# Kernel optimization log

Measured on AMD Instinct MI355X. Metric: run time of the kernel, lower is better.

Reference implementation:

```python
import jax, jax.numpy as jnp
import numpy as np

L, B, S, D = 12, 2, 2048, 768
QK, H, V = 128, 512, 32000
SCALE = 128 ** (-0.5)


def setup_inputs() -> dict:
    key = jax.random.key(0)
    ks = jax.random.split(key, 11)
    p = lambda k, shp: jax.random.normal(k, shp, dtype=jnp.float32) * 0.02
    return {
        "layer_outputs": jax.random.normal(ks[0], (L, B, S, D), dtype=jnp.float32),
        "Wq": p(ks[1], (D, QK)), "bq": jnp.zeros((QK,), jnp.float32),
        "Wk": p(ks[2], (D, QK)), "bk": jnp.zeros((QK,), jnp.float32),
        "Wv": p(ks[3], (D, H)),  "bv": jnp.zeros((H,), jnp.float32),
        "W1": p(ks[4], (H, H // 2)), "b1": jnp.zeros((H // 2,), jnp.float32),
        "W2": p(ks[5], (H // 2, V)), "b2": jnp.zeros((V,), jnp.float32),
    }


def reference(layer_outputs, Wq, bq, Wk, bk, Wv, bv, W1, b1, W2, b2):
    # layer_outputs: (L, B, S, D) -> h: (S, L, B, D) as in torch permute(2,0,1,3)
    h = jnp.transpose(layer_outputs, (2, 0, 1, 3))
    q_in = h.mean(axis=1)                              # (S, B, D)
    q = jax.nn.relu(q_in @ Wq + bq)                    # (S, B, 128)
    k = jax.nn.relu(h @ Wk + bk)                       # (S, L, B, 128)
    scores = jnp.einsum('sbd,slbd->slb', q, k)[..., None] * SCALE  # (S, L, B, 1)
    attn = jax.nn.softmax(scores, axis=1)              # softmax over layer axis
    v = h @ Wv + bv                                    # (S, L, B, H)
    agg = jnp.sum(attn * v, axis=1)                    # (S, B, H)
    agg = jnp.transpose(agg, (1, 0, 2))                # (B, S, H)
    mid = jax.nn.relu(agg @ W1 + b1)                   # (B, S, H//2); dropout is eval-mode identity
    return mid @ W2 + b2                               # (B, S, V)
```

## Files before the change

kernel.cpp:

```cpp
#include <hip/hip_runtime.h>

#define Snum 2048
#define SCALE 0.08838834764831845f

typedef __attribute__((ext_vector_type(8))) __bf16 bf16x8;
typedef __attribute__((ext_vector_type(4))) float f32x4;

__device__ inline unsigned short f2bf(float f) {
    unsigned int u = __float_as_uint(f);
    unsigned int r = u + 0x7FFFu + ((u >> 16) & 1u);
    return (unsigned short)(r >> 16);
}
__device__ inline float bf2f(unsigned short u) {
    return __uint_as_float(((unsigned)u) << 16);
}
__device__ inline void gld_lds16(const unsigned short* g, unsigned short* l) {
    __builtin_amdgcn_global_load_lds(
        (const __attribute__((address_space(1))) unsigned int*)g,
        (__attribute__((address_space(3))) unsigned int*)l, 16, 0, 0);
}

__global__ __launch_bounds__(256) void transpose_f2bf(
    const float* __restrict__ in, unsigned short* __restrict__ out, int K, int N)
{
    __shared__ float t[32][33];
    const int bx = blockIdx.x;
    const int by = blockIdx.y;
    const int tx = threadIdx.x & 31, ty = threadIdx.x >> 5;
    #pragma unroll
    for (int i = 0; i < 4; ++i) {
        int k = by * 32 + ty + i * 8, n = bx * 32 + tx;
        t[ty + i * 8][tx] = in[(size_t)k * N + n];
    }
    __syncthreads();
    #pragma unroll
    for (int i = 0; i < 4; ++i) {
        int n = bx * 32 + ty + i * 8, k = by * 32 + tx;
        out[(size_t)n * K + k] = f2bf(t[tx][ty + i * 8]);
    }
}

__global__ __launch_bounds__(256) void proj_qk(
    const float* __restrict__ x, const unsigned short* __restrict__ Bt,
    const float* __restrict__ bk,
    unsigned short* __restrict__ Kall,
    unsigned short* __restrict__ Pq)
{
    __shared__ __align__(16) unsigned short As[2][64 * 32];
    __shared__ __align__(16) unsigned short Bs[2][256 * 32];
    const int tid = threadIdx.x;
    const int wid = tid >> 6, lane = tid & 63;
    const int wn = wid * 64;
    const int lr = lane & 15, g = lane >> 4;
    const int r0 = blockIdx.x * 64;
    const int K = 768, NT = K / 32;

    const int arow = tid >> 2, akc = (tid & 3) * 8;

    f32x4 acc[4][4] = {};

    float4 a0 = *(const float4*)(x + (size_t)(r0 + arow) * K + akc);
    float4 a1 = *(const float4*)(x + (size_t)(r0 + arow) * K + akc + 4);
    {
        unsigned short v[8];
        v[0] = f2bf(a0.x); v[1] = f2bf(a0.y); v[2] = f2bf(a0.z); v[3] = f2bf(a0.w);
        v[4] = f2bf(a1.x); v[5] = f2bf(a1.y); v[6] = f2bf(a1.z); v[7] = f2bf(a1.w);
        *(uint4*)&As[0][arow * 32 + akc] = *(uint4*)v;
    }
    #pragma unroll
    for (int c = 0; c < 4; ++c) {
        int rr = wid * 64 + c * 16;
        gld_lds16(Bt + (size_t)(rr + (lane >> 2)) * K + (lane & 3) * 8, &Bs[0][rr * 32]);
    }
    __syncthreads();

    for (int t = 0; t < NT; ++t) {
        const int cur = t & 1, nxt = cur ^ 1;
        if (t + 1 < NT) {
            const int k0 = (t + 1) * 32;
            a0 = *(const float4*)(x + (size_t)(r0 + arow) * K + k0 + akc);
            a1 = *(const float4*)(x + (size_t)(r0 + arow) * K + k0 + akc + 4);
            #pragma unroll
            for (int c = 0; c < 4; ++c) {
                int rr = wid * 64 + c * 16;
                gld_lds16(Bt + (size_t)(rr + (lane >> 2)) * K + k0 + (lane & 3) * 8,
                          &Bs[nxt][rr * 32]);
            }
        }

        bf16x8 aF[4], bF[4];
        #pragma unroll
        for (int mm = 0; mm < 4; ++mm) aF[mm] = *(const bf16x8*)&As[cur][(mm * 16 + lr) * 32 + g * 8];
        #pragma unroll
        for (int nn = 0; nn < 4; ++nn) bF[nn] = *(const bf16x8*)&Bs[cur][(wn + nn * 16 + lr) * 32 + g * 8];
        #pragma unroll
        for (int mm = 0; mm < 4; ++mm)
            #pragma unroll
            for (int nn = 0; nn < 4; ++nn)
                acc[mm][nn] = __builtin_amdgcn_mfma_f32_16x16x32_bf16(aF[mm], bF[nn], acc[mm][nn], 0, 0, 0);

        if (t + 1 < NT) {
            unsigned short v[8];
            v[0] = f2bf(a0.x); v[1] = f2bf(a0.y); v[2] = f2bf(a0.z); v[3] = f2bf(a0.w);
            v[4] = f2bf(a1.x); v[5] = f2bf(a1.y); v[6] = f2bf(a1.z); v[7] = f2bf(a1.w);
            *(uint4*)&As[nxt][arow * 32 + akc] = *(uint4*)v;
        }
        __syncthreads();
    }

    #pragma unroll
    for (int mm = 0; mm < 4; ++mm)
        #pragma unroll
        for (int nn = 0; nn < 4; ++nn) {
            int col = wn + nn * 16 + lr;
            #pragma unroll
            for (int reg = 0; reg < 4; ++reg) {
                int orow = r0 + mm * 16 + g * 4 + reg;
                float v = acc[mm][nn][reg];
                if (col < 128) {
                    float kv = v + bk[col];
                    Kall[(size_t)orow * 128 + col] = f2bf(kv > 0.f ? kv : 0.f);
                } else {
                    Pq[(size_t)orow * 128 + (col - 128)] = f2bf(v);
                }
            }
        }
}

__global__ __launch_bounds__(256) void scores_hbar(
    const float* __restrict__ x,
    const unsigned short* __restrict__ Pq,
    const float* __restrict__ bq,
    const unsigned short* __restrict__ Kall,
    unsigned short* __restrict__ hbar)
{
    const int wid = threadIdx.x >> 6, lane = threadIdx.x & 63;
    const int r = blockIdx.x * 4 + wid;
    const int b = r >> 11, s = r & 2047;

    float qa = 0.f, qb_ = 0.f;
    #pragma unroll
    for (int l = 0; l < 12; ++l) {
        const unsigned short* prow = Pq + ((size_t)(l * 2 + b) * Snum + s) * 128 + lane * 2;
        unsigned int u = *(const unsigned int*)prow;
        qa += bf2f((unsigned short)(u & 0xFFFF));
        qb_ += bf2f((unsigned short)(u >> 16));
    }
    float q0 = qa * (1.0f / 12.0f) + bq[lane * 2];
    float q1 = qb_ * (1.0f / 12.0f) + bq[lane * 2 + 1];
    q0 = q0 > 0.f ? q0 : 0.f;
    q1 = q1 > 0.f ? q1 : 0.f;
    q0 = bf2f(f2bf(q0)); q1 = bf2f(f2bf(q1));

    float sc[12];
    #pragma unroll
    for (int l = 0; l < 12; ++l) {
        const unsigned short* krow = Kall + ((size_t)(l * 2 + b) * Snum + s) * 128 + lane * 2;
        unsigned int u = *(const unsigned int*)krow;
        float p = q0 * bf2f((unsigned short)(u & 0xFFFF)) + q1 * bf2f((unsigned short)(u >> 16));
        #pragma unroll
        for (int off = 32; off > 0; off >>= 1) p += __shfl_xor(p, off, 64);
        sc[l] = p * SCALE;
    }
    float m = sc[0];
    #pragma unroll
    for (int l = 1; l < 12; ++l) m = fmaxf(m, sc[l]);
    float att[12], den = 0.f;
    #pragma unroll
    for (int l = 0; l < 12; ++l) { att[l] = __expf(sc[l] - m); den += att[l]; }
    const float inv = 1.0f / den;
    #pragma unroll
    for (int l = 0; l < 12; ++l) att[l] *= inv;

    #pragma unroll
    for (int jv = 0; jv < 3; ++jv) {
        const int d0 = jv * 256 + lane * 4;
        float a0 = 0.f, a1 = 0.f, a2 = 0.f, a3 = 0.f;
        #pragma unroll
        for (int l = 0; l < 12; ++l) {
            const float4 v = *(const float4*)(x + ((size_t)(l * 2 + b) * Snum + s) * 768 + d0);
            a0 += att[l] * v.x; a1 += att[l] * v.y; a2 += att[l] * v.z; a3 += att[l] * v.w;
        }
        ushort4 o;
        o.x = f2bf(a0); o.y = f2bf(a1); o.z = f2bf(a2); o.w = f2bf(a3);
        *(ushort4*)(hbar + (size_t)r * 768 + d0) = o;
    }
}

template <int RELU, int OUT_BF16>
__global__ __launch_bounds__(256) void gemm64(
    const unsigned short* __restrict__ A, const unsigned short* __restrict__ Bt,
    const float* __restrict__ bias, void* __restrict__ out, int M, int N, int K)
{
    __shared__ __align__(16) unsigned short As[64][40];
    __shared__ __align__(16) unsigned short Bs[64][40];
    const int tid = threadIdx.x;
    const int bn = blockIdx.x, bm = blockIdx.y;
    const int wid = tid >> 6, lane = tid & 63;
    const int wm = (wid >> 1) * 32, wn = (wid & 1) * 32;
    const int lr = lane & 15, g = lane >> 4;
    const int r0 = bm * 64, c0 = bn * 64;

    f32x4 acc[2][2] = {};
    const int row = tid >> 2, kc = (tid & 3) * 8;

    for (int k0 = 0; k0 < K; k0 += 32) {
        __syncthreads();
        *(uint4*)&As[row][kc] = *(const uint4*)(A  + (size_t)(r0 + row) * K + k0 + kc);
        *(uint4*)&Bs[row][kc] = *(const uint4*)(Bt + (size_t)(c0 + row) * K + k0 + kc);
        __syncthreads();

        bf16x8 aF[2], bF[2];
        #pragma unroll
        for (int mm = 0; mm < 2; ++mm) aF[mm] = *(const bf16x8*)&As[wm + mm * 16 + lr][g * 8];
        #pragma unroll
        for (int nn = 0; nn < 2; ++nn) bF[nn] = *(const bf16x8*)&Bs[wn + nn * 16 + lr][g * 8];
        #pragma unroll
        for (int mm = 0; mm < 2; ++mm)
            #pragma unroll
            for (int nn = 0; nn < 2; ++nn)
                acc[mm][nn] = __builtin_amdgcn_mfma_f32_16x16x32_bf16(aF[mm], bF[nn], acc[mm][nn], 0, 0, 0);
    }

    #pragma unroll
    for (int mm = 0; mm < 2; ++mm)
        #pragma unroll
        for (int nn = 0; nn < 2; ++nn) {
            int col = c0 + wn + nn * 16 + lr;
            float bcol = bias[col];
            #pragma unroll
            for (int reg = 0; reg < 4; ++reg) {
                int orow = r0 + wm + mm * 16 + g * 4 + reg;
                float v = acc[mm][nn][reg] + bcol;
                if (RELU) v = v > 0.f ? v : 0.f;
                if (OUT_BF16) ((unsigned short*)out)[(size_t)orow * N + col] = f2bf(v);
                else          ((float*)out)[(size_t)orow * N + col] = v;
            }
        }
}

__global__ __launch_bounds__(256) void gemm_out(
    const unsigned short* __restrict__ A,
    const unsigned short* __restrict__ Bt,
    const float* __restrict__ bias, float* __restrict__ out)
{
    __shared__ __align__(16) unsigned short As[2][128 * 32];
    __shared__ __align__(16) unsigned short Bs[2][128 * 32];
    const int K = 256, N = 32000, NT = K / 32;
    const int orig = blockIdx.x;
    const int swz = (orig & 7) * 1000 + (orig >> 3);
    const int bn = swz >> 5;
    const int bm = swz & 31;
    const int tid = threadIdx.x;
    const int wid = tid >> 6, lane = tid & 63;
    const int wm = (wid >> 1) * 64, wn = (wid & 1) * 64;
    const int lr = lane & 15, g = lane >> 4;
    const int r0 = bm * 128, c0 = bn * 128;

    f32x4 acc[4][4] = {};

    #pragma unroll
    for (int c = 0; c < 2; ++c) {
        int rr = wid * 32 + c * 16;
        gld_lds16(A  + (size_t)(r0 + rr + (lane >> 2)) * K + (lane & 3) * 8, &As[0][rr * 32]);
        gld_lds16(Bt + (size_t)(c0 + rr + (lane >> 2)) * K + (lane & 3) * 8, &Bs[0][rr * 32]);
    }
    __syncthreads();

    for (int t = 0; t < NT; ++t) {
        const int cur = t & 1, nxt = cur ^ 1;
        if (t + 1 < NT) {
            const int k0 = (t + 1) * 32;
            #pragma unroll
            for (int c = 0; c < 2; ++c) {
                int rr = wid * 32 + c * 16;
                gld_lds16(A  + (size_t)(r0 + rr + (lane >> 2)) * K + k0 + (lane & 3) * 8, &As[nxt][rr * 32]);
                gld_lds16(Bt + (size_t)(c0 + rr + (lane >> 2)) * K + k0 + (lane & 3) * 8, &Bs[nxt][rr * 32]);
            }
        }

        bf16x8 aF[4], bF[4];
        #pragma unroll
        for (int mm = 0; mm < 4; ++mm) aF[mm] = *(const bf16x8*)&As[cur][(wm + mm * 16 + lr) * 32 + g * 8];
        #pragma unroll
        for (int nn = 0; nn < 4; ++nn) bF[nn] = *(const bf16x8*)&Bs[cur][(wn + nn * 16 + lr) * 32 + g * 8];
        #pragma unroll
        for (int mm = 0; mm < 4; ++mm)
            #pragma unroll
            for (int nn = 0; nn < 4; ++nn)
                acc[mm][nn] = __builtin_amdgcn_mfma_f32_16x16x32_bf16(aF[mm], bF[nn], acc[mm][nn], 0, 0, 0);
        __syncthreads();
    }

    #pragma unroll
    for (int mm = 0; mm < 4; ++mm)
        #pragma unroll
        for (int nn = 0; nn < 4; ++nn) {
            int col = c0 + wn + nn * 16 + lr;
            float bcol = bias[col];
            #pragma unroll
            for (int reg = 0; reg < 4; ++reg) {
                int orow = r0 + wm + mm * 16 + g * 4 + reg;
                out[(size_t)orow * N + col] = acc[mm][nn][reg] + bcol;
            }
        }
}

extern "C" void kernel_launch(void* const* d_in, const int* in_sizes, int n_in,
                              void* d_out, int out_size, void* d_ws, size_t ws_size,
                              hipStream_t stream) {
    (void)in_sizes; (void)n_in; (void)out_size; (void)ws_size;

    const float* x  = (const float*)d_in[0];
    const float* Wq = (const float*)d_in[1];
    const float* bq = (const float*)d_in[2];
    const float* Wk = (const float*)d_in[3];
    const float* bk = (const float*)d_in[4];
    const float* Wv = (const float*)d_in[5];
    const float* bv = (const float*)d_in[6];
    const float* W1 = (const float*)d_in[7];
    const float* b1 = (const float*)d_in[8];
    const float* W2 = (const float*)d_in[9];
    const float* b2 = (const float*)d_in[10];

    char* p = (char*)d_ws;
    unsigned short* Wqkt  = (unsigned short*)p; p += (size_t)256 * 768 * 2;
    unsigned short* Wvt   = (unsigned short*)p; p += (size_t)512 * 768 * 2;
    unsigned short* W1t   = (unsigned short*)p; p += (size_t)256 * 512 * 2;
    unsigned short* W2t   = (unsigned short*)p; p += (size_t)32000 * 256 * 2;
    unsigned short* Kall  = (unsigned short*)p; p += (size_t)49152 * 128 * 2;
    unsigned short* Pq    = (unsigned short*)p; p += (size_t)49152 * 128 * 2;
    unsigned short* hbar  = (unsigned short*)p; p += (size_t)4096 * 768 * 2;
    unsigned short* aggb  = (unsigned short*)p; p += (size_t)4096 * 512 * 2;
    unsigned short* midb  = (unsigned short*)p; p += (size_t)4096 * 256 * 2;

    transpose_f2bf<<<dim3(128 / 32, 768 / 32), dim3(256), 0, stream>>>(Wk, Wqkt, 768, 128);
    transpose_f2bf<<<dim3(128 / 32, 768 / 32), dim3(256), 0, stream>>>(Wq, Wqkt + (size_t)128 * 768, 768, 128);
    transpose_f2bf<<<dim3(512 / 32, 768 / 32), dim3(256), 0, stream>>>(Wv, Wvt, 768, 512);
    transpose_f2bf<<<dim3(256 / 32, 512 / 32), dim3(256), 0, stream>>>(W1, W1t, 512, 256);
    transpose_f2bf<<<dim3(32000 / 32, 256 / 32), dim3(256), 0, stream>>>(W2, W2t, 256, 32000);

    proj_qk<<<dim3(49152 / 64), dim3(256), 0, stream>>>(x, Wqkt, bk, Kall, Pq);

    scores_hbar<<<dim3(1024), dim3(256), 0, stream>>>(x, Pq, bq, Kall, hbar);

    gemm64<0, 1><<<dim3(512 / 64, 4096 / 64), dim3(256), 0, stream>>>(
        hbar, Wvt, bv, aggb, 4096, 512, 768);

    gemm64<1, 1><<<dim3(256 / 64, 4096 / 64), dim3(256), 0, stream>>>(
        aggb, W1t, b1, midb, 4096, 256, 512);

    gemm_out<<<dim3(8000), dim3(256), 0, stream>>>(midb, W2t, b2, (float*)d_out);
}
```

Measured before the change: 340.2 us.

## Merge weight transposes, swizzle LDS, swap MFMA operands for vector stores, deepen gemm_out K tile

Merges the five weight transpose launches into a single kernel that dispatches on block index. It XOR-swizzles the LDS layouts in proj_qk and gemm_out to reduce bank conflicts on fragment reads. Swapping the MFMA operand order makes each lane hold four consecutive output columns, so the epilogues write ushort4/float4 vectors instead of scalars. gemm_out also moves to a 64-wide K tile with four iterations, which doubles its LDS footprint and may lower occupancy.

```diff
diff --git a/kernel.cpp b/kernel.cpp
--- a/kernel.cpp
+++ b/kernel.cpp
@@ -20,12 +20,22 @@
         (__attribute__((address_space(3))) unsigned int*)l, 16, 0, 0);
 }
 
-__global__ __launch_bounds__(256) void transpose_f2bf(
-    const float* __restrict__ in, unsigned short* __restrict__ out, int K, int N)
+__global__ __launch_bounds__(256) void transpose_all(
+    const float* __restrict__ W2, unsigned short* __restrict__ W2t,
+    const float* __restrict__ Wv, unsigned short* __restrict__ Wvt,
+    const float* __restrict__ W1, unsigned short* __restrict__ W1t,
+    const float* __restrict__ Wk, const float* __restrict__ Wq,
+    unsigned short* __restrict__ Wqkt)
 {
     __shared__ float t[32][33];
-    const int bx = blockIdx.x;
-    const int by = blockIdx.y;
+    const int id = blockIdx.x;
+    const float* in; unsigned short* out; int K, N, bx, by;
+    if (id < 8000)      { in = W2; out = W2t;  K = 256; N = 32000; by = id & 7;  bx = id >> 3; }
+    else if (id < 8384) { int q = id - 8000; in = Wv; out = Wvt;  K = 768; N = 512; bx = q & 15; by = q >> 4; }
+    else if (id < 8512) { int q = id - 8384; in = W1; out = W1t;  K = 512; N = 256; bx = q & 7;  by = q >> 3; }
+    else if (id < 8608) { int q = id - 8512; in = Wk; out = Wqkt; K = 768; N = 128; bx = q & 3;  by = q >> 2; }
+    else                { int q = id - 8608; in = Wq; out = Wqkt + (size_t)128 * 768; K = 768; N = 128; bx = q & 3; by = q >> 2; }
+
     const int tx = threadIdx.x & 31, ty = threadIdx.x >> 5;
     #pragma unroll
     for (int i = 0; i < 4; ++i) {
@@ -55,22 +65,24 @@
     const int r0 = blockIdx.x * 64;
     const int K = 768, NT = K / 32;
 
-    const int arow = tid >> 2, akc = (tid & 3) * 8;
+    const int arow = tid >> 2;
+    const int aslot = (tid & 3) ^ (arow & 3);
+    const int bslot = (lane & 3) ^ ((lane >> 2) & 3);
 
     f32x4 acc[4][4] = {};
 
-    float4 a0 = *(const float4*)(x + (size_t)(r0 + arow) * K + akc);
-    float4 a1 = *(const float4*)(x + (size_t)(r0 + arow) * K + akc + 4);
+    float4 a0 = *(const float4*)(x + (size_t)(r0 + arow) * K + (tid & 3) * 8);
+    float4 a1 = *(const float4*)(x + (size_t)(r0 + arow) * K + (tid & 3) * 8 + 4);
     {
         unsigned short v[8];
         v[0] = f2bf(a0.x); v[1] = f2bf(a0.y); v[2] = f2bf(a0.z); v[3] = f2bf(a0.w);
         v[4] = f2bf(a1.x); v[5] = f2bf(a1.y); v[6] = f2bf(a1.z); v[7] = f2bf(a1.w);
-        *(uint4*)&As[0][arow * 32 + akc] = *(uint4*)v;
+        *(uint4*)&As[0][arow * 32 + aslot * 8] = *(uint4*)v;
     }
     #pragma unroll
     for (int c = 0; c < 4; ++c) {
         int rr = wid * 64 + c * 16;
-        gld_lds16(Bt + (size_t)(rr + (lane >> 2)) * K + (lane & 3) * 8, &Bs[0][rr * 32]);
+        gld_lds16(Bt + (size_t)(rr + (lane >> 2)) * K + bslot * 8, &Bs[0][rr * 32]);
     }
     __syncthreads();
 
@@ -78,32 +90,32 @@
         const int cur = t & 1, nxt = cur ^ 1;
         if (t + 1 < NT) {
             const int k0 = (t + 1) * 32;
-            a0 = *(const float4*)(x + (size_t)(r0 + arow) * K + k0 + akc);
-            a1 = *(const float4*)(x + (size_t)(r0 + arow) * K + k0 + akc + 4);
+            a0 = *(const float4*)(x + (size_t)(r0 + arow) * K + k0 + (tid & 3) * 8);
+            a1 = *(const float4*)(x + (size_t)(r0 + arow) * K + k0 + (tid & 3) * 8 + 4);
             #pragma unroll
             for (int c = 0; c < 4; ++c) {
                 int rr = wid * 64 + c * 16;
-                gld_lds16(Bt + (size_t)(rr + (lane >> 2)) * K + k0 + (lane & 3) * 8,
-                          &Bs[nxt][rr * 32]);
+                gld_lds16(Bt + (size_t)(rr + (lane >> 2)) * K + k0 + bslot * 8, &Bs[nxt][rr * 32]);
             }
         }
 
         bf16x8 aF[4], bF[4];
-        #pragma unroll
-        for (int mm = 0; mm < 4; ++mm) aF[mm] = *(const bf16x8*)&As[cur][(mm * 16 + lr) * 32 + g * 8];
-        #pragma unroll
-        for (int nn = 0; nn < 4; ++nn) bF[nn] = *(const bf16x8*)&Bs[cur][(wn + nn * 16 + lr) * 32 + g * 8];
+        const int rslot = (g ^ (lr & 3)) * 8;
+        #pragma unroll
+        for (int mm = 0; mm < 4; ++mm) aF[mm] = *(const bf16x8*)&As[cur][(mm * 16 + lr) * 32 + rslot];
+        #pragma unroll
+        for (int nn = 0; nn < 4; ++nn) bF[nn] = *(const bf16x8*)&Bs[cur][(wn + nn * 16 + lr) * 32 + rslot];
         #pragma unroll
         for (int mm = 0; mm < 4; ++mm)
             #pragma unroll
             for (int nn = 0; nn < 4; ++nn)
-                acc[mm][nn] = __builtin_amdgcn_mfma_f32_16x16x32_bf16(aF[mm], bF[nn], acc[mm][nn], 0, 0, 0);
+                acc[mm][nn] = __builtin_amdgcn_mfma_f32_16x16x32_bf16(bF[nn], aF[mm], acc[mm][nn], 0, 0, 0);
 
         if (t + 1 < NT) {
             unsigned short v[8];
             v[0] = f2bf(a0.x); v[1] = f2bf(a0.y); v[2] = f2bf(a0.z); v[3] = f2bf(a0.w);
             v[4] = f2bf(a1.x); v[5] = f2bf(a1.y); v[6] = f2bf(a1.z); v[7] = f2bf(a1.w);
-            *(uint4*)&As[nxt][arow * 32 + akc] = *(uint4*)v;
+            *(uint4*)&As[nxt][arow * 32 + aslot * 8] = *(uint4*)v;
         }
         __syncthreads();
     }
@@ -112,17 +124,20 @@
     for (int mm = 0; mm < 4; ++mm)
         #pragma unroll
         for (int nn = 0; nn < 4; ++nn) {
-            int col = wn + nn * 16 + lr;
-            #pragma unroll
-            for (int reg = 0; reg < 4; ++reg) {
-                int orow = r0 + mm * 16 + g * 4 + reg;
-                float v = acc[mm][nn][reg];
-                if (col < 128) {
-                    float kv = v + bk[col];
-                    Kall[(size_t)orow * 128 + col] = f2bf(kv > 0.f ? kv : 0.f);
-                } else {
-                    Pq[(size_t)orow * 128 + (col - 128)] = f2bf(v);
+            const int row = r0 + mm * 16 + lr;
+            const int colb = wn + nn * 16 + g * 4;
+            unsigned short o[4];
+            if (colb < 128) {
+                #pragma unroll
+                for (int reg = 0; reg < 4; ++reg) {
+                    float kv = acc[mm][nn][reg] + bk[colb + reg];
+                    o[reg] = f2bf(kv > 0.f ? kv : 0.f);
                 }
+                *(ushort4*)&Kall[(size_t)row * 128 + colb] = *(ushort4*)o;
+            } else {
+                #pragma unroll
+                for (int reg = 0; reg < 4; ++reg) o[reg] = f2bf(acc[mm][nn][reg]);
+                *(ushort4*)&Pq[(size_t)row * 128 + (colb - 128)] = *(ushort4*)o;
             }
         }
 }
@@ -219,22 +234,28 @@
         for (int mm = 0; mm < 2; ++mm)
             #pragma unroll
             for (int nn = 0; nn < 2; ++nn)
-                acc[mm][nn] = __builtin_amdgcn_mfma_f32_16x16x32_bf16(aF[mm], bF[nn], acc[mm][nn], 0, 0, 0);
+                acc[mm][nn] = __builtin_amdgcn_mfma_f32_16x16x32_bf16(bF[nn], aF[mm], acc[mm][nn], 0, 0, 0);
     }
 
     #pragma unroll
     for (int mm = 0; mm < 2; ++mm)
         #pragma unroll
         for (int nn = 0; nn < 2; ++nn) {
-            int col = c0 + wn + nn * 16 + lr;
-            float bcol = bias[col];
+            const int orow = r0 + wm + mm * 16 + lr;
+            const int colb = c0 + wn + nn * 16 + g * 4;
+            float vr[4];
             #pragma unroll
             for (int reg = 0; reg < 4; ++reg) {
-                int orow = r0 + wm + mm * 16 + g * 4 + reg;
-                float v = acc[mm][nn][reg] + bcol;
-                if (RELU) v = v > 0.f ? v : 0.f;
-                if (OUT_BF16) ((unsigned short*)out)[(size_t)orow * N + col] = f2bf(v);
-                else          ((float*)out)[(size_t)orow * N + col] = v;
+                float v = acc[mm][nn][reg] + bias[colb + reg];
+                vr[reg] = (RELU && v < 0.f) ? 0.f : v;
+            }
+            if (OUT_BF16) {
+                unsigned short o[4];
+                #pragma unroll
+                for (int reg = 0; reg < 4; ++reg) o[reg] = f2bf(vr[reg]);
+                *(ushort4*)&((unsigned short*)out)[(size_t)orow * N + colb] = *(ushort4*)o;
+            } else {
+                *(float4*)&((float*)out)[(size_t)orow * N + colb] = *(float4*)vr;
             }
         }
 }
@@ -244,51 +265,58 @@
     const unsigned short* __restrict__ Bt,
     const float* __restrict__ bias, float* __restrict__ out)
 {
-    __shared__ __align__(16) unsigned short As[2][128 * 32];
-    __shared__ __align__(16) unsigned short Bs[2][128 * 32];
-    const int K = 256, N = 32000, NT = K / 32;
+    __shared__ __align__(16) unsigned short As[2][128 * 64];
+    __shared__ __align__(16) unsigned short Bs[2][128 * 64];
+    const int K = 256, N = 32000, NT = 4;
     const int orig = blockIdx.x;
     const int swz = (orig & 7) * 1000 + (orig >> 3);
-    const int bn = swz >> 5;
-    const int bm = swz & 31;
+    const int bn = swz >> 5, bm = swz & 31;
     const int tid = threadIdx.x;
     const int wid = tid >> 6, lane = tid & 63;
     const int wm = (wid >> 1) * 64, wn = (wid & 1) * 64;
     const int lr = lane & 15, g = lane >> 4;
     const int r0 = bm * 128, c0 = bn * 128;
 
+    const int srow = lane >> 3;
+    const int kslot = (lane & 7) ^ (srow & 7);
+
     f32x4 acc[4][4] = {};
 
     #pragma unroll
-    for (int c = 0; c < 2; ++c) {
-        int rr = wid * 32 + c * 16;
-        gld_lds16(A  + (size_t)(r0 + rr + (lane >> 2)) * K + (lane & 3) * 8, &As[0][rr * 32]);
-        gld_lds16(Bt + (size_t)(c0 + rr + (lane >> 2)) * K + (lane & 3) * 8, &Bs[0][rr * 32]);
+    for (int c = 0; c < 4; ++c) {
+        const int rb = wid * 32 + c * 8;
+        gld_lds16(A  + (size_t)(r0 + rb + srow) * K + kslot * 8, &As[0][rb * 64]);
+        gld_lds16(Bt + (size_t)(c0 + rb + srow) * K + kslot * 8, &Bs[0][rb * 64]);
     }
     __syncthreads();
 
     for (int t = 0; t < NT; ++t) {
         const int cur = t & 1, nxt = cur ^ 1;
         if (t + 1 < NT) {
-            const int k0 = (t + 1) * 32;
-            #pragma unroll
-            for (int c = 0; c < 2; ++c) {
-                int rr = wid * 32 + c * 16;
-                gld_lds16(A  + (size_t)(r0 + rr + (lane >> 2)) * K + k0 + (lane & 3) * 8, &As[nxt][rr * 32]);
-                gld_lds16(Bt + (size_t)(c0 + rr + (lane >> 2)) * K + k0 + (lane & 3) * 8, &Bs[nxt][rr * 32]);
-            }
-        }
-
-        bf16x8 aF[4], bF[4];
-        #pragma unroll
-        for (int mm = 0; mm < 4; ++mm) aF[mm] = *(const bf16x8*)&As[cur][(wm + mm * 16 + lr) * 32 + g * 8];
-        #pragma unroll
-        for (int nn = 0; nn < 4; ++nn) bF[nn] = *(const bf16x8*)&Bs[cur][(wn + nn * 16 + lr) * 32 + g * 8];
-        #pragma unroll
-        for (int mm = 0; mm < 4; ++mm)
+            const int k0 = (t + 1) * 64;
+            #pragma unroll
+            for (int c = 0; c < 4; ++c) {
+                const int rb = wid * 32 + c * 8;
+                gld_lds16(A  + (size_t)(r0 + rb + srow) * K + k0 + kslot * 8, &As[nxt][rb * 64]);
+                gld_lds16(Bt + (size_t)(c0 + rb + srow) * K + k0 + kslot * 8, &Bs[nxt][rb * 64]);
+            }
+        }
+
+        #pragma unroll
+        for (int kk = 0; kk < 2; ++kk) {
+            bf16x8 aF[4], bF[4];
+            #pragma unroll
+            for (int mm = 0; mm < 4; ++mm)
+                aF[mm] = *(const bf16x8*)&As[cur][(wm + mm * 16 + lr) * 64 + (((kk * 4 + g) ^ (lr & 7)) * 8)];
             #pragma unroll
             for (int nn = 0; nn < 4; ++nn)
-                acc[mm][nn] = __builtin_amdgcn_mfma_f32_16x16x32_bf16(aF[mm], bF[nn], acc[mm][nn], 0, 0, 0);
+                bF[nn] = *(const bf16x8*)&Bs[cur][(wn + nn * 16 + lr) * 64 + (((kk * 4 + g) ^ (lr & 7)) * 8)];
+            #pragma unroll
+            for (int mm = 0; mm < 4; ++mm)
+                #pragma unroll
+                for (int nn = 0; nn < 4; ++nn)
+                    acc[mm][nn] = __builtin_amdgcn_mfma_f32_16x16x32_bf16(bF[nn], aF[mm], acc[mm][nn], 0, 0, 0);
+        }
         __syncthreads();
     }
 
@@ -296,13 +324,15 @@
     for (int mm = 0; mm < 4; ++mm)
         #pragma unroll
         for (int nn = 0; nn < 4; ++nn) {
-            int col = c0 + wn + nn * 16 + lr;
-            float bcol = bias[col];
-            #pragma unroll
-            for (int reg = 0; reg < 4; ++reg) {
-                int orow = r0 + wm + mm * 16 + g * 4 + reg;
-                out[(size_t)orow * N + col] = acc[mm][nn][reg] + bcol;
-            }
+            const int row = r0 + wm + mm * 16 + lr;
+            const int colb = c0 + wn + nn * 16 + g * 4;
+            const float4 b4 = *(const float4*)&bias[colb];
+            float o[4];
+            o[0] = acc[mm][nn][0] + b4.x;
+            o[1] = acc[mm][nn][1] + b4.y;
+            o[2] = acc[mm][nn][2] + b4.z;
+            o[3] = acc[mm][nn][3] + b4.w;
+            *(float4*)&out[(size_t)row * N + colb] = *(float4*)o;
         }
 }
 
@@ -334,11 +364,8 @@
     unsigned short* aggb  = (unsigned short*)p; p += (size_t)4096 * 512 * 2;
     unsigned short* midb  = (unsigned short*)p; p += (size_t)4096 * 256 * 2;
 
-    transpose_f2bf<<<dim3(128 / 32, 768 / 32), dim3(256), 0, stream>>>(Wk, Wqkt, 768, 128);
-    transpose_f2bf<<<dim3(128 / 32, 768 / 32), dim3(256), 0, stream>>>(Wq, Wqkt + (size_t)128 * 768, 768, 128);
-    transpose_f2bf<<<dim3(512 / 32, 768 / 32), dim3(256), 0, stream>>>(Wv, Wvt, 768, 512);
-    transpose_f2bf<<<dim3(256 / 32, 512 / 32), dim3(256), 0, stream>>>(W1, W1t, 512, 256);
-    transpose_f2bf<<<dim3(32000 / 32, 256 / 32), dim3(256), 0, stream>>>(W2, W2t, 256, 32000);
+    transpose_all<<<dim3(8704), dim3(256), 0, stream>>>(
+        W2, W2t, Wv, Wvt, W1, W1t, Wk, Wq, Wqkt);
 
     proj_qk<<<dim3(49152 / 64), dim3(256), 0, stream>>>(x, Wqkt, bk, Kall, Pq);
 
```

Result: slower. 378.3 us (+11.2%).

## Merge weight transposes, enlarge proj_qk tile, and vectorize GEMM epilogue stores

Applied to the files above, without the earlier changes.

Merges four small weight-transpose kernels into one launch and folds the large W2 transpose into the scores kernel as extra blocks, cutting launch count and letting that transpose overlap the scores work. proj_qk moves to 128-row tiles with 512 threads, so each Wqk tile loaded into LDS serves more rows. The MFMA operands are swapped in all GEMMs so each lane holds four consecutive output columns, which allows ushort4/float4 stores. The final logits are written with nontemporal stores. The risks are lower occupancy from the bigger proj_qk block and a lopsided mix of block types in the merged scores launch.

```diff
diff --git a/kernel.cpp b/kernel.cpp
--- a/kernel.cpp
+++ b/kernel.cpp
@@ -20,12 +20,20 @@
         (__attribute__((address_space(3))) unsigned int*)l, 16, 0, 0);
 }
 
-__global__ __launch_bounds__(256) void transpose_f2bf(
-    const float* __restrict__ in, unsigned short* __restrict__ out, int K, int N)
+__global__ __launch_bounds__(256) void transpose_small(
+    const float* __restrict__ Wv, unsigned short* __restrict__ Wvt,
+    const float* __restrict__ W1, unsigned short* __restrict__ W1t,
+    const float* __restrict__ Wk, const float* __restrict__ Wq,
+    unsigned short* __restrict__ Wqkt)
 {
     __shared__ float t[32][33];
-    const int bx = blockIdx.x;
-    const int by = blockIdx.y;
+    const int id = blockIdx.x;
+    const float* in; unsigned short* out; int K, N, bx, by;
+    if (id < 384)      { int q = id;       in = Wv; out = Wvt;  K = 768; N = 512; bx = q & 15; by = q >> 4; }
+    else if (id < 512) { int q = id - 384; in = W1; out = W1t;  K = 512; N = 256; bx = q & 7;  by = q >> 3; }
+    else if (id < 608) { int q = id - 512; in = Wk; out = Wqkt; K = 768; N = 128; bx = q & 3;  by = q >> 2; }
+    else               { int q = id - 608; in = Wq; out = Wqkt + (size_t)128 * 768; K = 768; N = 128; bx = q & 3; by = q >> 2; }
+
     const int tx = threadIdx.x & 31, ty = threadIdx.x >> 5;
     #pragma unroll
     for (int i = 0; i < 4; ++i) {
@@ -40,20 +48,20 @@
     }
 }
 
-__global__ __launch_bounds__(256) void proj_qk(
+__global__ __launch_bounds__(512) void proj_qk(
     const float* __restrict__ x, const unsigned short* __restrict__ Bt,
     const float* __restrict__ bk,
     unsigned short* __restrict__ Kall,
     unsigned short* __restrict__ Pq)
 {
-    __shared__ __align__(16) unsigned short As[2][64 * 32];
+    __shared__ __align__(16) unsigned short As[2][128 * 32];
     __shared__ __align__(16) unsigned short Bs[2][256 * 32];
     const int tid = threadIdx.x;
     const int wid = tid >> 6, lane = tid & 63;
-    const int wn = wid * 64;
+    const int wm = (wid >> 2) * 64, wn = (wid & 3) * 64;
     const int lr = lane & 15, g = lane >> 4;
-    const int r0 = blockIdx.x * 64;
-    const int K = 768, NT = K / 32;
+    const int r0 = blockIdx.x * 128;
+    const int K = 768, NT = 24;
 
     const int arow = tid >> 2, akc = (tid & 3) * 8;
 
@@ -68,8 +76,8 @@
         *(uint4*)&As[0][arow * 32 + akc] = *(uint4*)v;
     }
     #pragma unroll
-    for (int c = 0; c < 4; ++c) {
-        int rr = wid * 64 + c * 16;
+    for (int c = 0; c < 2; ++c) {
+        int rr = wid * 32 + c * 16;
         gld_lds16(Bt + (size_t)(rr + (lane >> 2)) * K + (lane & 3) * 8, &Bs[0][rr * 32]);
     }
     __syncthreads();
@@ -81,8 +89,8 @@
             a0 = *(const float4*)(x + (size_t)(r0 + arow) * K + k0 + akc);
             a1 = *(const float4*)(x + (size_t)(r0 + arow) * K + k0 + akc + 4);
             #pragma unroll
-            for (int c = 0; c < 4; ++c) {
-                int rr = wid * 64 + c * 16;
+            for (int c = 0; c < 2; ++c) {
+                int rr = wid * 32 + c * 16;
                 gld_lds16(Bt + (size_t)(rr + (lane >> 2)) * K + k0 + (lane & 3) * 8,
                           &Bs[nxt][rr * 32]);
             }
@@ -90,14 +98,14 @@
 
         bf16x8 aF[4], bF[4];
         #pragma unroll
-        for (int mm = 0; mm < 4; ++mm) aF[mm] = *(const bf16x8*)&As[cur][(mm * 16 + lr) * 32 + g * 8];
+        for (int mm = 0; mm < 4; ++mm) aF[mm] = *(const bf16x8*)&As[cur][(wm + mm * 16 + lr) * 32 + g * 8];
         #pragma unroll
         for (int nn = 0; nn < 4; ++nn) bF[nn] = *(const bf16x8*)&Bs[cur][(wn + nn * 16 + lr) * 32 + g * 8];
         #pragma unroll
         for (int mm = 0; mm < 4; ++mm)
             #pragma unroll
             for (int nn = 0; nn < 4; ++nn)
-                acc[mm][nn] = __builtin_amdgcn_mfma_f32_16x16x32_bf16(aF[mm], bF[nn], acc[mm][nn], 0, 0, 0);
+                acc[mm][nn] = __builtin_amdgcn_mfma_f32_16x16x32_bf16(bF[nn], aF[mm], acc[mm][nn], 0, 0, 0);
 
         if (t + 1 < NT) {
             unsigned short v[8];
@@ -112,28 +120,51 @@
     for (int mm = 0; mm < 4; ++mm)
         #pragma unroll
         for (int nn = 0; nn < 4; ++nn) {
-            int col = wn + nn * 16 + lr;
-            #pragma unroll
-            for (int reg = 0; reg < 4; ++reg) {
-                int orow = r0 + mm * 16 + g * 4 + reg;
-                float v = acc[mm][nn][reg];
-                if (col < 128) {
-                    float kv = v + bk[col];
-                    Kall[(size_t)orow * 128 + col] = f2bf(kv > 0.f ? kv : 0.f);
-                } else {
-                    Pq[(size_t)orow * 128 + (col - 128)] = f2bf(v);
+            const int row = r0 + wm + mm * 16 + lr;
+            const int colb = wn + nn * 16 + g * 4;
+            unsigned short o[4];
+            if (colb < 128) {
+                #pragma unroll
+                for (int reg = 0; reg < 4; ++reg) {
+                    float kv = acc[mm][nn][reg] + bk[colb + reg];
+                    o[reg] = f2bf(kv > 0.f ? kv : 0.f);
                 }
-            }
-        }
-}
-
-__global__ __launch_bounds__(256) void scores_hbar(
+                *(ushort4*)&Kall[(size_t)row * 128 + colb] = *(ushort4*)o;
+            } else {
+                #pragma unroll
+                for (int reg = 0; reg < 4; ++reg) o[reg] = f2bf(acc[mm][nn][reg]);
+                *(ushort4*)&Pq[(size_t)row * 128 + (colb - 128)] = *(ushort4*)o;
+            }
+        }
+}
+
+__global__ __launch_bounds__(256) void scores_plus_w2t(
     const float* __restrict__ x,
     const unsigned short* __restrict__ Pq,
     const float* __restrict__ bq,
     const unsigned short* __restrict__ Kall,
-    unsigned short* __restrict__ hbar)
-{
+    unsigned short* __restrict__ hbar,
+    const float* __restrict__ W2, unsigned short* __restrict__ W2t)
+{
+    if (blockIdx.x >= 1024) {
+        __shared__ float t[32][33];
+        const int id = blockIdx.x - 1024;
+        const int bx = id >> 3, by = id & 7;
+        const int tx = threadIdx.x & 31, ty = threadIdx.x >> 5;
+        #pragma unroll
+        for (int i = 0; i < 4; ++i) {
+            int k = by * 32 + ty + i * 8, n = bx * 32 + tx;
+            t[ty + i * 8][tx] = W2[(size_t)k * 32000 + n];
+        }
+        __syncthreads();
+        #pragma unroll
+        for (int i = 0; i < 4; ++i) {
+            int n = bx * 32 + ty + i * 8, k = by * 32 + tx;
+            W2t[(size_t)n * 256 + k] = f2bf(t[tx][ty + i * 8]);
+        }
+        return;
+    }
+
     const int wid = threadIdx.x >> 6, lane = threadIdx.x & 63;
     const int r = blockIdx.x * 4 + wid;
     const int b = r >> 11, s = r & 2047;
@@ -219,22 +250,28 @@
         for (int mm = 0; mm < 2; ++mm)
             #pragma unroll
             for (int nn = 0; nn < 2; ++nn)
-                acc[mm][nn] = __builtin_amdgcn_mfma_f32_16x16x32_bf16(aF[mm], bF[nn], acc[mm][nn], 0, 0, 0);
+                acc[mm][nn] = __builtin_amdgcn_mfma_f32_16x16x32_bf16(bF[nn], aF[mm], acc[mm][nn], 0, 0, 0);
     }
 
     #pragma unroll
     for (int mm = 0; mm < 2; ++mm)
         #pragma unroll
         for (int nn = 0; nn < 2; ++nn) {
-            int col = c0 + wn + nn * 16 + lr;
-            float bcol = bias[col];
+            const int orow = r0 + wm + mm * 16 + lr;
+            const int colb = c0 + wn + nn * 16 + g * 4;
+            float vr[4];
             #pragma unroll
             for (int reg = 0; reg < 4; ++reg) {
-                int orow = r0 + wm + mm * 16 + g * 4 + reg;
-                float v = acc[mm][nn][reg] + bcol;
-                if (RELU) v = v > 0.f ? v : 0.f;
-                if (OUT_BF16) ((unsigned short*)out)[(size_t)orow * N + col] = f2bf(v);
-                else          ((float*)out)[(size_t)orow * N + col] = v;
+                float v = acc[mm][nn][reg] + bias[colb + reg];
+                vr[reg] = (RELU && v < 0.f) ? 0.f : v;
+            }
+            if (OUT_BF16) {
+                unsigned short o[4];
+                #pragma unroll
+                for (int reg = 0; reg < 4; ++reg) o[reg] = f2bf(vr[reg]);
+                *(ushort4*)&((unsigned short*)out)[(size_t)orow * N + colb] = *(ushort4*)o;
+            } else {
+                *(float4*)&((float*)out)[(size_t)orow * N + colb] = *(float4*)vr;
             }
         }
 }
@@ -246,11 +283,10 @@
 {
     __shared__ __align__(16) unsigned short As[2][128 * 32];
     __shared__ __align__(16) unsigned short Bs[2][128 * 32];
-    const int K = 256, N = 32000, NT = K / 32;
+    const int K = 256, N = 32000, NT = 8;
     const int orig = blockIdx.x;
     const int swz = (orig & 7) * 1000 + (orig >> 3);
-    const int bn = swz >> 5;
-    const int bm = swz & 31;
+    const int bn = swz >> 5, bm = swz & 31;
     const int tid = threadIdx.x;
     const int wid = tid >> 6, lane = tid & 63;
     const int wm = (wid >> 1) * 64, wn = (wid & 1) * 64;
@@ -288,7 +324,7 @@
         for (int mm = 0; mm < 4; ++mm)
             #pragma unroll
             for (int nn = 0; nn < 4; ++nn)
-                acc[mm][nn] = __builtin_amdgcn_mfma_f32_16x16x32_bf16(aF[mm], bF[nn], acc[mm][nn], 0, 0, 0);
+                acc[mm][nn] = __builtin_amdgcn_mfma_f32_16x16x32_bf16(bF[nn], aF[mm], acc[mm][nn], 0, 0, 0);
         __syncthreads();
     }
 
@@ -296,13 +332,12 @@
     for (int mm = 0; mm < 4; ++mm)
         #pragma unroll
         for (int nn = 0; nn < 4; ++nn) {
-            int col = c0 + wn + nn * 16 + lr;
-            float bcol = bias[col];
-            #pragma unroll
-            for (int reg = 0; reg < 4; ++reg) {
-                int orow = r0 + wm + mm * 16 + g * 4 + reg;
-                out[(size_t)orow * N + col] = acc[mm][nn][reg] + bcol;
-            }
+            const int row = r0 + wm + mm * 16 + lr;
+            const int colb = c0 + wn + nn * 16 + g * 4;
+            const float4 b4 = *(const float4*)&bias[colb];
+            f32x4 o = acc[mm][nn];
+            o[0] += b4.x; o[1] += b4.y; o[2] += b4.z; o[3] += b4.w;
+            __builtin_nontemporal_store(o, (f32x4*)&out[(size_t)row * N + colb]);
         }
 }
 
@@ -334,15 +369,12 @@
     unsigned short* aggb  = (unsigned short*)p; p += (size_t)4096 * 512 * 2;
     unsigned short* midb  = (unsigned short*)p; p += (size_t)4096 * 256 * 2;
 
-    transpose_f2bf<<<dim3(128 / 32, 768 / 32), dim3(256), 0, stream>>>(Wk, Wqkt, 768, 128);
-    transpose_f2bf<<<dim3(128 / 32, 768 / 32), dim3(256), 0, stream>>>(Wq, Wqkt + (size_t)128 * 768, 768, 128);
-    transpose_f2bf<<<dim3(512 / 32, 768 / 32), dim3(256), 0, stream>>>(Wv, Wvt, 768, 512);
-    transpose_f2bf<<<dim3(256 / 32, 512 / 32), dim3(256), 0, stream>>>(W1, W1t, 512, 256);
-    transpose_f2bf<<<dim3(32000 / 32, 256 / 32), dim3(256), 0, stream>>>(W2, W2t, 256, 32000);
-
-    proj_qk<<<dim3(49152 / 64), dim3(256), 0, stream>>>(x, Wqkt, bk, Kall, Pq);
-
-    scores_hbar<<<dim3(1024), dim3(256), 0, stream>>>(x, Pq, bq, Kall, hbar);
+    transpose_small<<<dim3(704), dim3(256), 0, stream>>>(Wv, Wvt, W1, W1t, Wk, Wq, Wqkt);
+
+    proj_qk<<<dim3(49152 / 128), dim3(512), 0, stream>>>(x, Wqkt, bk, Kall, Pq);
+
+    scores_plus_w2t<<<dim3(1024 + 8000), dim3(256), 0, stream>>>(
+        x, Pq, bq, Kall, hbar, W2, W2t);
 
     gemm64<0, 1><<<dim3(512 / 64, 4096 / 64), dim3(256), 0, stream>>>(
         hbar, Wvt, bv, aggb, 4096, 512, 768);
```

Result: faster. 281.7 us (-17.2%).
